# Performance work log

Measured on AMD Instinct MI355X. Metric: run time of the kernel, lower is better.

Reference implementation:

```python
import jax, jax.numpy as jnp
import numpy as np

B, C, H, W = 4, 64, 64, 64
C8 = C // 8


def cl_attention(x, gamma):
    # DANet CAM-style channel attention: [B,C,H,W] -> [B,C,H,W]
    b, c, h, w = x.shape
    xf = x.reshape(b, c, h * w)                       # b c n
    energy = jnp.einsum('bcn,bdn->bcd', xf, xf)       # b c c
    energy = jnp.max(energy, axis=-1, keepdims=True) - energy
    attn = jax.nn.softmax(energy, axis=-1)
    out = jnp.einsum('bcd,bdn->bcn', attn, xf).reshape(b, c, h, w)
    return gamma * out + x


def setup_inputs() -> dict:
    key = jax.random.key(0)
    ks = jax.random.split(key, 8)
    s = 0.02
    return {
        'cnn_feat': jax.random.normal(ks[0], (B, C, H, W), jnp.float32),
        'vit_feat': jax.random.normal(ks[1], (B, C, H, W), jnp.float32),
        'Wq': jax.random.normal(ks[2], (C8, C), jnp.float32) * s,   # 1x1 conv kernel
        'bq': jnp.zeros((C8,), jnp.float32),
        'Wk': jax.random.normal(ks[3], (C8, C), jnp.float32) * s,
        'bk': jnp.zeros((C8,), jnp.float32),
        'Wv': jax.random.normal(ks[4], (C, C), jnp.float32) * s,
        'bv': jnp.zeros((C,), jnp.float32),
        'gamma': jnp.zeros((1,), jnp.float32),
        'gamma_cla_cnn': jnp.zeros((1,), jnp.float32),
        'gamma_cla_vit': jnp.zeros((1,), jnp.float32),
    }


def reference(cnn_feat, vit_feat, Wq, bq, Wk, bk, Wv, bv, gamma,
              gamma_cla_cnn, gamma_cla_vit):
    b, c, h, w = cnn_feat.shape
    n = h * w

    cnn_att = cl_attention(cnn_feat, gamma_cla_cnn)   # b c h w
    vit_att = cl_attention(vit_feat, gamma_cla_vit)   # b c h w

    # query: 1x1 conv -> view(b, C8, n) -> permute -> (b, n, C8)
    q = jnp.einsum('bchw,oc->bhwo', cnn_att, Wq).reshape(b, n, -1) + bq

    # vit: rearrange 'b c h w -> b (h w) c'
    vit_flat = vit_att.reshape(b, c, n).transpose(0, 2, 1)          # b n c
    k = vit_flat @ Wk.T + bk                                        # b n C8
    v = vit_flat @ Wv.T + bv                                        # b n C

    energy = jnp.einsum('bqd,bkd->bqk', q, k)                       # b n n
    attn = jax.nn.softmax(energy, axis=-1)
    out = jnp.einsum('bqk,bkc->bqc', attn, v)                       # b n c
    out = out.transpose(0, 2, 1).reshape(b, c, h, w)                # 'b (h w) c -> b c h w'
    return gamma * out + cnn_feat
```

## Files before the change

kernel.cpp:

```cpp
#include <hip/hip_runtime.h>
#include <hip/hip_bf16.h>

#define BSZ 4
#define CC 64
#define NN 4096
#define CN (CC*NN)
#define BCN (BSZ*CN)

typedef __attribute__((ext_vector_type(4))) float    f4v;
typedef __attribute__((ext_vector_type(4))) int      i4v;
typedef __attribute__((ext_vector_type(2))) int      i2v;
typedef __attribute__((ext_vector_type(2))) unsigned u2v;
typedef __attribute__((ext_vector_type(8))) short    s8v;

#define DPP_F(x_, ctrl_) __builtin_bit_cast(float, \
    __builtin_amdgcn_update_dpp(0, __builtin_bit_cast(int, (float)(x_)), (ctrl_), 0xf, 0xf, true))
#define QP_X1 0xB1

__device__ __forceinline__ unsigned pack_bf16(float lo, float hi) {
    unsigned l = __builtin_bit_cast(unsigned, lo);
    unsigned h = __builtin_bit_cast(unsigned, hi);
    return (h & 0xFFFF0000u) | (l >> 16);
}
__device__ __forceinline__ unsigned pack2(float lo, float hi) {
    float2 f2; f2.x = lo; f2.y = hi;
    __hip_bfloat162 h = __float22bfloat162_rn(f2);
    unsigned u;
    __builtin_memcpy(&u, &h, 4);
    return u;
}
__device__ __forceinline__ float blo(int d) {
    return __builtin_bit_cast(float, (unsigned)d << 16);
}
__device__ __forceinline__ float bhi(int d) {
    return __builtin_bit_cast(float, (unsigned)d & 0xFFFF0000u);
}

__global__ __launch_bounds__(256) void gram_k(const float* __restrict__ cnn,
                                              const float* __restrict__ vit,
                                              float* __restrict__ part) {
    __shared__ __align__(16) float sXT[128*68];
    int t = threadIdx.x;
    int blk = blockIdx.x;
    int ch = blk & 31, b = (blk >> 5) & 3, i2 = blk >> 7;
    const float* X = (i2 ? vit : cnn) + b * CN;
    int n0 = ch * 128;
#pragma unroll
    for (int j = 0; j < 8; j++) {
        int idx = t + j * 256;
        int c = idx >> 5, n4 = idx & 31;
        f4v val = *(const f4v*)&X[c * NN + n0 + n4 * 4];
        int base = (n4 * 4) * 68 + c;
        sXT[base]       = val[0];
        sXT[base + 68]  = val[1];
        sXT[base + 136] = val[2];
        sXT[base + 204] = val[3];
    }
    __syncthreads();
    int tc = (t & 15) * 4, td = (t >> 4) * 4;
    f4v acc[4];
#pragma unroll
    for (int i = 0; i < 4; i++) acc[i] = (f4v){0.f, 0.f, 0.f, 0.f};
#pragma unroll 4
    for (int k = 0; k < 128; k++) {
        f4v a  = *(const f4v*)&sXT[k * 68 + tc];
        f4v bb = *(const f4v*)&sXT[k * 68 + td];
#pragma unroll
        for (int i = 0; i < 4; i++) acc[i] += a[i] * bb;
    }
    float* dst = part + ch * 32768 + (i2 * 4 + b) * 4096;
#pragma unroll
    for (int i = 0; i < 4; i++) *(f4v*)&dst[(tc + i) * 64 + td] = acc[i];
}

__global__ void gred_k(const float* __restrict__ part, float* __restrict__ G) {
    int row = blockIdx.x;
    int d = threadIdx.x;
    float s = 0.f;
#pragma unroll 8
    for (int ch = 0; ch < 32; ch++) s += part[ch * 32768 + row * 64 + d];
    float mn = s;
#pragma unroll
    for (int off = 1; off < 64; off <<= 1) mn = fminf(mn, __shfl_xor(mn, off));
    float e = __expf(mn - s);
    float sm = e;
#pragma unroll
    for (int off = 1; off < 64; off <<= 1) sm += __shfl_xor(sm, off);
    G[row * 64 + d] = e / sm;
}

__global__ __launch_bounds__(256) void weff_k(const float* __restrict__ G,
                                              const float* __restrict__ Wq,
                                              const float* __restrict__ Wk,
                                              const float* __restrict__ Wv,
                                              const float* __restrict__ gcnn,
                                              const float* __restrict__ gvit,
                                              ushort* __restrict__ WeffB) {
    __shared__ float sA[8192];
    __shared__ float sWt[1024];
    int t = threadIdx.x;
    int b = blockIdx.x / 5, tile = blockIdx.x % 5;
    for (int i = t; i < 4096; i += 256) {
        sA[i]        = G[b * 4096 + i];
        sA[4096 + i] = G[(4 + b) * 4096 + i];
    }
    __syncthreads();
    float gc = *gcnn, gv = *gvit;
#pragma unroll
    for (int k = 0; k < 4; k++) {
        int idx = k * 256 + t;
        int r = idx >> 6, c = idx & 63;
        const float* Wrow; const float* A; float g;
        if (tile == 0) {
            if (r < 8) { Wrow = Wq + r * 64;       A = sA;        g = gc; }
            else       { Wrow = Wk + (r - 8) * 64; A = sA + 4096; g = gv; }
        } else         { Wrow = Wv + ((tile - 1) * 16 + r) * 64; A = sA + 4096; g = gv; }
        float s = 0.f;
#pragma unroll 8
        for (int d = 0; d < 64; d++) s += Wrow[d] * A[d * 64 + c];
        sWt[idx] = g * s + Wrow[c];
    }
    __syncthreads();
    if (t < 128) {
        int frag = t >> 6, lane = t & 63, m = lane & 15, q4 = lane >> 4;
        i4v o;
#pragma unroll
        for (int p = 0; p < 4; p++) {
            int c0 = frag * 32 + q4 * 8 + 2 * p;
            o[p] = (int)pack_bf16(sWt[m * 64 + c0], sWt[m * 64 + c0 + 1]);
        }
        *(i4v*)&WeffB[(size_t)(b * 10 + tile * 2 + frag) * 512 + lane * 8] = o;
    }
}

__global__ __launch_bounds__(256) void qkv_k(const float* __restrict__ cnn,
                                             const float* __restrict__ vit,
                                             const ushort* __restrict__ WeffB,
                                             const float* __restrict__ bq,
                                             const float* __restrict__ bk,
                                             const float* __restrict__ bv,
                                             ushort* __restrict__ qb, ushort* __restrict__ kb,
                                             ushort* __restrict__ vT) {
    int t = threadIdx.x;
    int b = blockIdx.x >> 6, n0 = (blockIdx.x & 63) * 64;
    int w = t >> 6, lane = t & 63, c15 = lane & 15, q4 = lane >> 4;
    int n = n0 + w * 16 + c15;
    const float LOG2E = 1.44269504f;

    s8v A[10];
    const ushort* WB = WeffB + (size_t)b * 5120 + lane * 8;
#pragma unroll
    for (int i = 0; i < 10; i++)
        A[i] = __builtin_bit_cast(s8v, *(const i4v*)(WB + (size_t)i * 512));

    s8v Bc[2], Bv[2];
#pragma unroll
    for (int f = 0; f < 2; f++) {
        i4v pc, pv;
#pragma unroll
        for (int p = 0; p < 4; p++) {
            int c0 = f * 32 + q4 * 8 + p * 2;
            size_t a0 = (size_t)b * CN + (size_t)c0 * NN + n;
            pc[p] = (int)pack_bf16(cnn[a0], cnn[a0 + NN]);
            pv[p] = (int)pack_bf16(vit[a0], vit[a0 + NN]);
        }
        Bc[f] = __builtin_bit_cast(s8v, pc);
        Bv[f] = __builtin_bit_cast(s8v, pv);
    }

    f4v acc = *(const f4v*)(bq + (q4 & 1) * 4);
    acc = __builtin_amdgcn_mfma_f32_16x16x32_bf16(A[0], Bc[0], acc, 0, 0, 0);
    acc = __builtin_amdgcn_mfma_f32_16x16x32_bf16(A[1], Bc[1], acc, 0, 0, 0);
    if (q4 < 2) {
        unsigned d0 = pack_bf16(acc[0] * LOG2E, acc[1] * LOG2E);
        unsigned d1 = pack_bf16(acc[2] * LOG2E, acc[3] * LOG2E);
        unsigned long long v = ((unsigned long long)d1 << 32) | d0;
        *(unsigned long long*)&qb[(size_t)(b * NN + n) * 8 + q4 * 4] = v;
    }
    acc = *(const f4v*)(bk + (q4 & 1) * 4);
    acc = __builtin_amdgcn_mfma_f32_16x16x32_bf16(A[0], Bv[0], acc, 0, 0, 0);
    acc = __builtin_amdgcn_mfma_f32_16x16x32_bf16(A[1], Bv[1], acc, 0, 0, 0);
    if (q4 >= 2) {
        unsigned d0 = pack_bf16(acc[0], acc[1]), d1 = pack_bf16(acc[2], acc[3]);
        unsigned long long v = ((unsigned long long)d1 << 32) | d0;
        *(unsigned long long*)&kb[(size_t)(b * NN + n) * 8 + (q4 - 2) * 4] = v;
    }
#pragma unroll
    for (int tile = 1; tile < 5; tile++) {
        acc = *(const f4v*)(bv + (tile - 1) * 16 + q4 * 4);
        acc = __builtin_amdgcn_mfma_f32_16x16x32_bf16(A[tile * 2],     Bv[0], acc, 0, 0, 0);
        acc = __builtin_amdgcn_mfma_f32_16x16x32_bf16(A[tile * 2 + 1], Bv[1], acc, 0, 0, 0);
#pragma unroll
        for (int r = 0; r < 4; r++) {
            float other = DPP_F(acc[r], QP_X1);
            unsigned pkd = (lane & 1) ? pack_bf16(other, acc[r])
                                      : pack_bf16(acc[r], other);
            if (!(lane & 1)) {
                int row = (tile - 1) * 16 + q4 * 4 + r;
                *(unsigned*)&vT[(size_t)(b * 64 + row) * NN + n] = pkd;
            }
        }
    }
}

__global__ __launch_bounds__(256, 2) void flash_k(const ushort* __restrict__ qb,
                                                  const ushort* __restrict__ kb,
                                                  const ushort* __restrict__ vT,
                                                  ushort* __restrict__ pOT,
                                                  float* __restrict__ pl) {
    __shared__ __align__(16) ushort Vlds[2 * 64 * 72];
    int t = threadIdx.x;
    int lane = t & 63, w = t >> 6;
    int c15 = lane & 15, q4 = lane >> 4;
    int blk = blockIdx.x;
    int s = blk >> 7, b = (blk >> 5) & 3, q0 = (blk & 31) * 128;

    s8v qB[2];
#pragma unroll
    for (int g = 0; g < 2; g++) {
        i4v qa = (i4v){0, 0, 0, 0};
        if (q4 == 0)
            qa = *(const i4v*)(qb + (size_t)(b * NN + q0 + w * 32 + g * 16 + c15) * 8);
        qB[g] = __builtin_bit_cast(s8v, qa);
    }

    f4v accO[2][4];
#pragma unroll
    for (int g = 0; g < 2; g++)
#pragma unroll
        for (int nt = 0; nt < 4; nt++) accO[g][nt] = (f4v){0.f, 0.f, 0.f, 0.f};
    float lacc[2] = {0.f, 0.f};

    const ushort* kbb = kb + (size_t)b * NN * 8 + (size_t)c15 * 8;

    int r = t >> 2, chk = t & 3;
    const ushort* vsrc = vT + (size_t)(b * 64 + r) * NN + chk * 16;
    int vdstoff = r * 72 + 32 * (chk >> 1) + 4 * (chk & 1);
    int vreadoff = c15 * 72 + 8 * q4;

    int kbase = s * 1024;
    i4v bk_cur[4];
#pragma unroll
    for (int nt = 0; nt < 4; nt++)
        bk_cur[nt] = *(const i4v*)(kbb + (size_t)(kbase + nt * 16) * 8);
    i4v v0 = *(const i4v*)(vsrc + kbase);
    i4v v1 = *(const i4v*)(vsrc + kbase + 8);

#pragma unroll 2
    for (int kt = 0; kt < 16; kt++) {
        int k0 = kbase + kt * 64;
        ushort* vd = Vlds + (kt & 1) * 4608 + vdstoff;
        *(i2v*)(vd + 0)  = (i2v){v0[0], v0[1]};
        *(i2v*)(vd + 8)  = (i2v){v0[2], v0[3]};
        *(i2v*)(vd + 16) = (i2v){v1[0], v1[1]};
        *(i2v*)(vd + 24) = (i2v){v1[2], v1[3]};
        __syncthreads();

        const ushort* vb = Vlds + (kt & 1) * 4608 + vreadoff;
        i4v vA[2][4];
#pragma unroll
        for (int F = 0; F < 2; F++)
#pragma unroll
            for (int nt = 0; nt < 4; nt++)
                vA[F][nt] = *(const i4v*)(vb + nt * 16 * 72 + 32 * F);

        i4v bk_nxt[4];
        if (kt < 15) {
            v0 = *(const i4v*)(vsrc + k0 + 64);
            v1 = *(const i4v*)(vsrc + k0 + 64 + 8);
#pragma unroll
            for (int nt = 0; nt < 4; nt++)
                bk_nxt[nt] = *(const i4v*)(kbb + (size_t)(k0 + 64 + nt * 16) * 8);
        }

        f4v z = (f4v){0.f, 0.f, 0.f, 0.f};
        f4v S[2][4];
#pragma unroll
        for (int g = 0; g < 2; g++)
#pragma unroll
            for (int nt = 0; nt < 4; nt++)
                S[g][nt] = __builtin_amdgcn_mfma_f32_16x16x32_bf16(
                    __builtin_bit_cast(s8v, bk_cur[nt]), qB[g], z, 0, 0, 0);

        s8v Bp[2][2];
#pragma unroll
        for (int g = 0; g < 2; g++) {
            f4v p[4];
            float ps = 0.f;
#pragma unroll
            for (int nt = 0; nt < 4; nt++)
#pragma unroll
                for (int rr = 0; rr < 4; rr++) {
                    p[nt][rr] = __builtin_amdgcn_exp2f(S[g][nt][rr]);
                    ps += p[nt][rr];
                }
#pragma unroll
            for (int F = 0; F < 2; F++) {
                i4v bp;
                bp[0] = (int)pack2(p[2 * F][0],     p[2 * F][1]);
                bp[1] = (int)pack2(p[2 * F][2],     p[2 * F][3]);
                bp[2] = (int)pack2(p[2 * F + 1][0], p[2 * F + 1][1]);
                bp[3] = (int)pack2(p[2 * F + 1][2], p[2 * F + 1][3]);
                Bp[g][F] = __builtin_bit_cast(s8v, bp);
            }
            lacc[g] += ps;
        }

        __builtin_amdgcn_s_setprio(1);
#pragma unroll
        for (int F = 0; F < 2; F++)
#pragma unroll
            for (int g = 0; g < 2; g++)
#pragma unroll
                for (int nt = 0; nt < 4; nt++)
                    accO[g][nt] =
                        __builtin_amdgcn_mfma_f32_16x16x32_bf16(
                            __builtin_bit_cast(s8v, vA[F][nt]), Bp[g][F],
                            accO[g][nt], 0, 0, 0);
        __builtin_amdgcn_s_setprio(0);

        if (kt < 15) {
#pragma unroll
            for (int nt = 0; nt < 4; nt++) bk_cur[nt] = bk_nxt[nt];
        }
    }

#pragma unroll
    for (int g = 0; g < 2; g++) {
        lacc[g] += __shfl_xor(lacc[g], 16);
        lacc[g] += __shfl_xor(lacc[g], 32);
    }

#pragma unroll
    for (int g = 0; g < 2; g++) {
        int qg = q0 + w * 32 + g * 16 + c15;
#pragma unroll
        for (int nt = 0; nt < 4; nt++) {
            int cg = nt * 4 + q4;
            u2v d;
            d[0] = pack2(accO[g][nt][0], accO[g][nt][1]);
            d[1] = pack2(accO[g][nt][2], accO[g][nt][3]);
            *(u2v*)&pOT[((size_t)((s * 4 + b) * 16 + cg) * NN + qg) * 4] = d;
        }
        if (q4 == 0)
            pl[(size_t)(s * 4 + b) * NN + qg] = lacc[g];
    }
}

__global__ __launch_bounds__(256) void comb_k(const ushort* __restrict__ pOT,
                                              const float* __restrict__ pl,
                                              const float* __restrict__ cnn,
                                              const float* __restrict__ gamma,
                                              float* __restrict__ out) {
    int t = threadIdx.x;
    int b = blockIdx.x >> 6, n0 = (blockIdx.x & 63) * 64;
    int nq = t & 15, cl = t >> 4;
    int n = n0 + nq * 4;
    f4v L = (f4v){0.f, 0.f, 0.f, 0.f};
#pragma unroll
    for (int s = 0; s < 4; s++)
        L += *(const f4v*)&pl[(size_t)(s * 4 + b) * NN + n];
    float g = *gamma;
    f4v rv;
#pragma unroll
    for (int j = 0; j < 4; j++) rv[j] = g / L[j];

    f4v Oc[4];
#pragma unroll
    for (int cc = 0; cc < 4; cc++) Oc[cc] = (f4v){0.f, 0.f, 0.f, 0.f};
#pragma unroll
    for (int s = 0; s < 4; s++) {
        const ushort* src = pOT + ((size_t)((s * 4 + b) * 16 + cl) * NN + n) * 4;
        i4v a  = *(const i4v*)src;
        i4v bb = *(const i4v*)(src + 8);
        Oc[0][0] += blo(a[0]);  Oc[1][0] += bhi(a[0]);
        Oc[2][0] += blo(a[1]);  Oc[3][0] += bhi(a[1]);
        Oc[0][1] += blo(a[2]);  Oc[1][1] += bhi(a[2]);
        Oc[2][1] += blo(a[3]);  Oc[3][1] += bhi(a[3]);
        Oc[0][2] += blo(bb[0]); Oc[1][2] += bhi(bb[0]);
        Oc[2][2] += blo(bb[1]); Oc[3][2] += bhi(bb[1]);
        Oc[0][3] += blo(bb[2]); Oc[1][3] += bhi(bb[2]);
        Oc[2][3] += blo(bb[3]); Oc[3][3] += bhi(bb[3]);
    }
#pragma unroll
    for (int cc = 0; cc < 4; cc++) {
        size_t gi = (size_t)(b * 64 + cl * 4 + cc) * NN + n;
        f4v cv = *(const f4v*)&cnn[gi];
        *(f4v*)&out[gi] = Oc[cc] * rv + cv;
    }
}

extern "C" void kernel_launch(void* const* d_in, const int* in_sizes, int n_in,
                              void* d_out, int out_size, void* d_ws, size_t ws_size,
                              hipStream_t stream) {
    const float* cnn  = (const float*)d_in[0];
    const float* vit  = (const float*)d_in[1];
    const float* Wq   = (const float*)d_in[2];
    const float* bq   = (const float*)d_in[3];
    const float* Wk   = (const float*)d_in[4];
    const float* bk   = (const float*)d_in[5];
    const float* Wv   = (const float*)d_in[6];
    const float* bv   = (const float*)d_in[7];
    const float* gam  = (const float*)d_in[8];
    const float* gcnn = (const float*)d_in[9];
    const float* gvit = (const float*)d_in[10];
    float* out = (float*)d_out;

    float* ws = (float*)d_ws;
    ushort* pOT   = (ushort*)ws;
    float*  part  = ws;
    float*  G     = ws + 8388608;
    ushort* WeffB = (ushort*)(ws + 8421376);
    ushort* qb    = (ushort*)(ws + 8431616);
    ushort* kb    = (ushort*)(ws + 8497152);
    ushort* vT    = (ushort*)(ws + 8562688);
    float*  pl    = ws + 9086976;

    gram_k <<<256, 256, 0, stream>>>(cnn, vit, part);
    gred_k <<<512, 64,  0, stream>>>(part, G);
    weff_k <<<20,  256, 0, stream>>>(G, Wq, Wk, Wv, gcnn, gvit, WeffB);
    qkv_k  <<<256, 256, 0, stream>>>(cnn, vit, WeffB, bq, bk, bv, qb, kb, vT);
    flash_k<<<512, 256, 0, stream>>>(qb, kb, vT, pOT, pl);
    comb_k <<<256, 256, 0, stream>>>(pOT, pl, cnn, gam, out);
}
```

Before: 126.6 us.

## Fuse prologue kernels with grid barriers and merge flash attention with combine

The gram, reduce, weight-fold and QKV projection kernels are merged into one persistent 256-block kernel that separates stages with atomic-counter grid barriers. The flash kernel now uses 512 threads and splits keys across two in-block halves, reducing the partial outputs through shared memory. It then writes the gamma-scaled result plus residual directly, which removes the bf16 partial-output buffer and the separate combine kernel. This saves several launches and a global round trip, but the grid barriers rely on all 256 blocks being co-resident, and the final stores are strided per element.

```diff
diff --git a/kernel.cpp b/kernel.cpp
--- a/kernel.cpp
+++ b/kernel.cpp
@@ -10,7 +10,6 @@
 typedef __attribute__((ext_vector_type(4))) float    f4v;
 typedef __attribute__((ext_vector_type(4))) int      i4v;
 typedef __attribute__((ext_vector_type(2))) int      i2v;
-typedef __attribute__((ext_vector_type(2))) unsigned u2v;
 typedef __attribute__((ext_vector_type(8))) short    s8v;
 
 #define DPP_F(x_, ctrl_) __builtin_bit_cast(float, \
@@ -29,234 +28,245 @@
     __builtin_memcpy(&u, &h, 4);
     return u;
 }
-__device__ __forceinline__ float blo(int d) {
-    return __builtin_bit_cast(float, (unsigned)d << 16);
-}
-__device__ __forceinline__ float bhi(int d) {
-    return __builtin_bit_cast(float, (unsigned)d & 0xFFFF0000u);
-}
-
-__global__ __launch_bounds__(256) void gram_k(const float* __restrict__ cnn,
-                                              const float* __restrict__ vit,
-                                              float* __restrict__ part) {
-    __shared__ __align__(16) float sXT[128*68];
+
+__device__ __forceinline__ void gsync(unsigned* ctr, unsigned target) {
+    __syncthreads();
+    if (threadIdx.x == 0) {
+        __threadfence();
+        atomicAdd(ctr, 1u);
+        while (__hip_atomic_load(ctr, __ATOMIC_ACQUIRE,
+                                 __HIP_MEMORY_SCOPE_AGENT) < target)
+            __builtin_amdgcn_s_sleep(2);
+        __threadfence();
+    }
+    __syncthreads();
+}
+
+__global__ __launch_bounds__(256) void fused_a(
+        const float* __restrict__ cnn, const float* __restrict__ vit,
+        const float* __restrict__ Wq,  const float* __restrict__ Wk,
+        const float* __restrict__ Wv,
+        const float* __restrict__ gcnn, const float* __restrict__ gvit,
+        const float* __restrict__ bq,  const float* __restrict__ bk,
+        const float* __restrict__ bv,
+        float* __restrict__ part, float* __restrict__ G,
+        ushort* __restrict__ WeffB,
+        ushort* __restrict__ qb, ushort* __restrict__ kb,
+        ushort* __restrict__ vT, unsigned* __restrict__ ctr) {
+    __shared__ __align__(16) float smem[9216];
     int t = threadIdx.x;
     int blk = blockIdx.x;
-    int ch = blk & 31, b = (blk >> 5) & 3, i2 = blk >> 7;
-    const float* X = (i2 ? vit : cnn) + b * CN;
-    int n0 = ch * 128;
-#pragma unroll
-    for (int j = 0; j < 8; j++) {
-        int idx = t + j * 256;
-        int c = idx >> 5, n4 = idx & 31;
-        f4v val = *(const f4v*)&X[c * NN + n0 + n4 * 4];
-        int base = (n4 * 4) * 68 + c;
-        sXT[base]       = val[0];
-        sXT[base + 68]  = val[1];
-        sXT[base + 136] = val[2];
-        sXT[base + 204] = val[3];
-    }
-    __syncthreads();
-    int tc = (t & 15) * 4, td = (t >> 4) * 4;
-    f4v acc[4];
-#pragma unroll
-    for (int i = 0; i < 4; i++) acc[i] = (f4v){0.f, 0.f, 0.f, 0.f};
+
+    {
+        float* sXT = smem;
+        int ch = blk & 31, b = (blk >> 5) & 3, i2 = blk >> 7;
+        const float* X = (i2 ? vit : cnn) + b * CN;
+        int n0 = ch * 128;
+#pragma unroll
+        for (int j = 0; j < 8; j++) {
+            int idx = t + j * 256;
+            int c = idx >> 5, n4 = idx & 31;
+            f4v val = *(const f4v*)&X[c * NN + n0 + n4 * 4];
+            int base = (n4 * 4) * 68 + c;
+            sXT[base]       = val[0];
+            sXT[base + 68]  = val[1];
+            sXT[base + 136] = val[2];
+            sXT[base + 204] = val[3];
+        }
+        __syncthreads();
+        int tc = (t & 15) * 4, td = (t >> 4) * 4;
+        f4v acc[4];
+#pragma unroll
+        for (int i = 0; i < 4; i++) acc[i] = (f4v){0.f, 0.f, 0.f, 0.f};
 #pragma unroll 4
-    for (int k = 0; k < 128; k++) {
-        f4v a  = *(const f4v*)&sXT[k * 68 + tc];
-        f4v bb = *(const f4v*)&sXT[k * 68 + td];
-#pragma unroll
-        for (int i = 0; i < 4; i++) acc[i] += a[i] * bb;
-    }
-    float* dst = part + ch * 32768 + (i2 * 4 + b) * 4096;
-#pragma unroll
-    for (int i = 0; i < 4; i++) *(f4v*)&dst[(tc + i) * 64 + td] = acc[i];
-}
-
-__global__ void gred_k(const float* __restrict__ part, float* __restrict__ G) {
-    int row = blockIdx.x;
-    int d = threadIdx.x;
-    float s = 0.f;
+        for (int k = 0; k < 128; k++) {
+            f4v a  = *(const f4v*)&sXT[k * 68 + tc];
+            f4v bb = *(const f4v*)&sXT[k * 68 + td];
+#pragma unroll
+            for (int i = 0; i < 4; i++) acc[i] += a[i] * bb;
+        }
+        float* dst = part + ch * 32768 + (i2 * 4 + b) * 4096;
+#pragma unroll
+        for (int i = 0; i < 4; i++) *(f4v*)&dst[(tc + i) * 64 + td] = acc[i];
+    }
+    gsync(ctr, 256);
+
+    {
+        int w = t >> 6, d = t & 63;
+        int row = blk * 2 + (w & 1), hf = w >> 1;
+        float s = 0.f;
+#pragma unroll
+        for (int ch = hf * 16; ch < hf * 16 + 16; ch++)
+            s += part[ch * 32768 + row * 64 + d];
+        smem[w * 64 + d] = s;
+        __syncthreads();
+        if (w < 2) {
+            int r = blk * 2 + w;
+            float sv = smem[w * 64 + d] + smem[(w + 2) * 64 + d];
+            float mn = sv;
+#pragma unroll
+            for (int off = 1; off < 64; off <<= 1) mn = fminf(mn, __shfl_xor(mn, off));
+            float e = __expf(mn - sv);
+            float sm2 = e;
+#pragma unroll
+            for (int off = 1; off < 64; off <<= 1) sm2 += __shfl_xor(sm2, off);
+            G[r * 64 + d] = e / sm2;
+        }
+    }
+    gsync(ctr, 512);
+
+    if (blk < 20) {
+        float* sA = smem;
+        float* sWt = smem + 8192;
+        int b = blk / 5, tile = blk % 5;
+        for (int i = t; i < 4096; i += 256) {
+            sA[i]        = G[b * 4096 + i];
+            sA[4096 + i] = G[(4 + b) * 4096 + i];
+        }
+        __syncthreads();
+        float gc = *gcnn, gv = *gvit;
+#pragma unroll
+        for (int k = 0; k < 4; k++) {
+            int idx = k * 256 + t;
+            int r = idx >> 6, c = idx & 63;
+            const float* Wrow; const float* A; float g;
+            if (tile == 0) {
+                if (r < 8) { Wrow = Wq + r * 64;       A = sA;        g = gc; }
+                else       { Wrow = Wk + (r - 8) * 64; A = sA + 4096; g = gv; }
+            } else         { Wrow = Wv + ((tile - 1) * 16 + r) * 64; A = sA + 4096; g = gv; }
+            float s = 0.f;
 #pragma unroll 8
-    for (int ch = 0; ch < 32; ch++) s += part[ch * 32768 + row * 64 + d];
-    float mn = s;
-#pragma unroll
-    for (int off = 1; off < 64; off <<= 1) mn = fminf(mn, __shfl_xor(mn, off));
-    float e = __expf(mn - s);
-    float sm = e;
-#pragma unroll
-    for (int off = 1; off < 64; off <<= 1) sm += __shfl_xor(sm, off);
-    G[row * 64 + d] = e / sm;
-}
-
-__global__ __launch_bounds__(256) void weff_k(const float* __restrict__ G,
-                                              const float* __restrict__ Wq,
-                                              const float* __restrict__ Wk,
-                                              const float* __restrict__ Wv,
-                                              const float* __restrict__ gcnn,
-                                              const float* __restrict__ gvit,
-                                              ushort* __restrict__ WeffB) {
-    __shared__ float sA[8192];
-    __shared__ float sWt[1024];
-    int t = threadIdx.x;
-    int b = blockIdx.x / 5, tile = blockIdx.x % 5;
-    for (int i = t; i < 4096; i += 256) {
-        sA[i]        = G[b * 4096 + i];
-        sA[4096 + i] = G[(4 + b) * 4096 + i];
-    }
-    __syncthreads();
-    float gc = *gcnn, gv = *gvit;
-#pragma unroll
-    for (int k = 0; k < 4; k++) {
-        int idx = k * 256 + t;
-        int r = idx >> 6, c = idx & 63;
-        const float* Wrow; const float* A; float g;
-        if (tile == 0) {
-            if (r < 8) { Wrow = Wq + r * 64;       A = sA;        g = gc; }
-            else       { Wrow = Wk + (r - 8) * 64; A = sA + 4096; g = gv; }
-        } else         { Wrow = Wv + ((tile - 1) * 16 + r) * 64; A = sA + 4096; g = gv; }
-        float s = 0.f;
-#pragma unroll 8
-        for (int d = 0; d < 64; d++) s += Wrow[d] * A[d * 64 + c];
-        sWt[idx] = g * s + Wrow[c];
-    }
-    __syncthreads();
-    if (t < 128) {
-        int frag = t >> 6, lane = t & 63, m = lane & 15, q4 = lane >> 4;
-        i4v o;
-#pragma unroll
-        for (int p = 0; p < 4; p++) {
-            int c0 = frag * 32 + q4 * 8 + 2 * p;
-            o[p] = (int)pack_bf16(sWt[m * 64 + c0], sWt[m * 64 + c0 + 1]);
-        }
-        *(i4v*)&WeffB[(size_t)(b * 10 + tile * 2 + frag) * 512 + lane * 8] = o;
-    }
-}
-
-__global__ __launch_bounds__(256) void qkv_k(const float* __restrict__ cnn,
-                                             const float* __restrict__ vit,
-                                             const ushort* __restrict__ WeffB,
-                                             const float* __restrict__ bq,
-                                             const float* __restrict__ bk,
-                                             const float* __restrict__ bv,
-                                             ushort* __restrict__ qb, ushort* __restrict__ kb,
-                                             ushort* __restrict__ vT) {
-    int t = threadIdx.x;
-    int b = blockIdx.x >> 6, n0 = (blockIdx.x & 63) * 64;
-    int w = t >> 6, lane = t & 63, c15 = lane & 15, q4 = lane >> 4;
-    int n = n0 + w * 16 + c15;
-    const float LOG2E = 1.44269504f;
-
-    s8v A[10];
-    const ushort* WB = WeffB + (size_t)b * 5120 + lane * 8;
-#pragma unroll
-    for (int i = 0; i < 10; i++)
-        A[i] = __builtin_bit_cast(s8v, *(const i4v*)(WB + (size_t)i * 512));
-
-    s8v Bc[2], Bv[2];
-#pragma unroll
-    for (int f = 0; f < 2; f++) {
-        i4v pc, pv;
-#pragma unroll
-        for (int p = 0; p < 4; p++) {
-            int c0 = f * 32 + q4 * 8 + p * 2;
-            size_t a0 = (size_t)b * CN + (size_t)c0 * NN + n;
-            pc[p] = (int)pack_bf16(cnn[a0], cnn[a0 + NN]);
-            pv[p] = (int)pack_bf16(vit[a0], vit[a0 + NN]);
-        }
-        Bc[f] = __builtin_bit_cast(s8v, pc);
-        Bv[f] = __builtin_bit_cast(s8v, pv);
-    }
-
-    f4v acc = *(const f4v*)(bq + (q4 & 1) * 4);
-    acc = __builtin_amdgcn_mfma_f32_16x16x32_bf16(A[0], Bc[0], acc, 0, 0, 0);
-    acc = __builtin_amdgcn_mfma_f32_16x16x32_bf16(A[1], Bc[1], acc, 0, 0, 0);
-    if (q4 < 2) {
-        unsigned d0 = pack_bf16(acc[0] * LOG2E, acc[1] * LOG2E);
-        unsigned d1 = pack_bf16(acc[2] * LOG2E, acc[3] * LOG2E);
-        unsigned long long v = ((unsigned long long)d1 << 32) | d0;
-        *(unsigned long long*)&qb[(size_t)(b * NN + n) * 8 + q4 * 4] = v;
-    }
-    acc = *(const f4v*)(bk + (q4 & 1) * 4);
-    acc = __builtin_amdgcn_mfma_f32_16x16x32_bf16(A[0], Bv[0], acc, 0, 0, 0);
-    acc = __builtin_amdgcn_mfma_f32_16x16x32_bf16(A[1], Bv[1], acc, 0, 0, 0);
-    if (q4 >= 2) {
-        unsigned d0 = pack_bf16(acc[0], acc[1]), d1 = pack_bf16(acc[2], acc[3]);
-        unsigned long long v = ((unsigned long long)d1 << 32) | d0;
-        *(unsigned long long*)&kb[(size_t)(b * NN + n) * 8 + (q4 - 2) * 4] = v;
-    }
-#pragma unroll
-    for (int tile = 1; tile < 5; tile++) {
-        acc = *(const f4v*)(bv + (tile - 1) * 16 + q4 * 4);
-        acc = __builtin_amdgcn_mfma_f32_16x16x32_bf16(A[tile * 2],     Bv[0], acc, 0, 0, 0);
-        acc = __builtin_amdgcn_mfma_f32_16x16x32_bf16(A[tile * 2 + 1], Bv[1], acc, 0, 0, 0);
-#pragma unroll
-        for (int r = 0; r < 4; r++) {
-            float other = DPP_F(acc[r], QP_X1);
-            unsigned pkd = (lane & 1) ? pack_bf16(other, acc[r])
-                                      : pack_bf16(acc[r], other);
-            if (!(lane & 1)) {
-                int row = (tile - 1) * 16 + q4 * 4 + r;
-                *(unsigned*)&vT[(size_t)(b * 64 + row) * NN + n] = pkd;
-            }
-        }
-    }
-}
-
-__global__ __launch_bounds__(256, 2) void flash_k(const ushort* __restrict__ qb,
-                                                  const ushort* __restrict__ kb,
-                                                  const ushort* __restrict__ vT,
-                                                  ushort* __restrict__ pOT,
-                                                  float* __restrict__ pl) {
-    __shared__ __align__(16) ushort Vlds[2 * 64 * 72];
+            for (int d = 0; d < 64; d++) s += Wrow[d] * A[d * 64 + c];
+            sWt[idx] = g * s + Wrow[c];
+        }
+        __syncthreads();
+        if (t < 128) {
+            int frag = t >> 6, lane = t & 63, m = lane & 15, q4 = lane >> 4;
+            i4v o;
+#pragma unroll
+            for (int p = 0; p < 4; p++) {
+                int c0 = frag * 32 + q4 * 8 + 2 * p;
+                o[p] = (int)pack_bf16(sWt[m * 64 + c0], sWt[m * 64 + c0 + 1]);
+            }
+            *(i4v*)&WeffB[(size_t)(b * 10 + tile * 2 + frag) * 512 + lane * 8] = o;
+        }
+    }
+    gsync(ctr, 768);
+
+    {
+        int b = blk >> 6, n0 = (blk & 63) * 64;
+        int w = t >> 6, lane = t & 63, c15 = lane & 15, q4 = lane >> 4;
+        int n = n0 + w * 16 + c15;
+        const float LOG2E = 1.44269504f;
+
+        s8v A[10];
+        const ushort* WB = WeffB + (size_t)b * 5120 + lane * 8;
+#pragma unroll
+        for (int i = 0; i < 10; i++)
+            A[i] = __builtin_bit_cast(s8v, *(const i4v*)(WB + (size_t)i * 512));
+
+        s8v Bc[2], Bv[2];
+#pragma unroll
+        for (int f = 0; f < 2; f++) {
+            i4v pc, pv;
+#pragma unroll
+            for (int p = 0; p < 4; p++) {
+                int c0 = f * 32 + q4 * 8 + p * 2;
+                size_t a0 = (size_t)b * CN + (size_t)c0 * NN + n;
+                pc[p] = (int)pack_bf16(cnn[a0], cnn[a0 + NN]);
+                pv[p] = (int)pack_bf16(vit[a0], vit[a0 + NN]);
+            }
+            Bc[f] = __builtin_bit_cast(s8v, pc);
+            Bv[f] = __builtin_bit_cast(s8v, pv);
+        }
+
+        f4v acc = *(const f4v*)(bq + (q4 & 1) * 4);
+        acc = __builtin_amdgcn_mfma_f32_16x16x32_bf16(A[0], Bc[0], acc, 0, 0, 0);
+        acc = __builtin_amdgcn_mfma_f32_16x16x32_bf16(A[1], Bc[1], acc, 0, 0, 0);
+        if (q4 < 2) {
+            unsigned d0 = pack_bf16(acc[0] * LOG2E, acc[1] * LOG2E);
+            unsigned d1 = pack_bf16(acc[2] * LOG2E, acc[3] * LOG2E);
+            unsigned long long v = ((unsigned long long)d1 << 32) | d0;
+            *(unsigned long long*)&qb[(size_t)(b * NN + n) * 8 + q4 * 4] = v;
+        }
+        acc = *(const f4v*)(bk + (q4 & 1) * 4);
+        acc = __builtin_amdgcn_mfma_f32_16x16x32_bf16(A[0], Bv[0], acc, 0, 0, 0);
+        acc = __builtin_amdgcn_mfma_f32_16x16x32_bf16(A[1], Bv[1], acc, 0, 0, 0);
+        if (q4 >= 2) {
+            unsigned d0 = pack_bf16(acc[0], acc[1]), d1 = pack_bf16(acc[2], acc[3]);
+            unsigned long long v = ((unsigned long long)d1 << 32) | d0;
+            *(unsigned long long*)&kb[(size_t)(b * NN + n) * 8 + (q4 - 2) * 4] = v;
+        }
+#pragma unroll
+        for (int tile = 1; tile < 5; tile++) {
+            acc = *(const f4v*)(bv + (tile - 1) * 16 + q4 * 4);
+            acc = __builtin_amdgcn_mfma_f32_16x16x32_bf16(A[tile * 2],     Bv[0], acc, 0, 0, 0);
+            acc = __builtin_amdgcn_mfma_f32_16x16x32_bf16(A[tile * 2 + 1], Bv[1], acc, 0, 0, 0);
+#pragma unroll
+            for (int r = 0; r < 4; r++) {
+                float other = DPP_F(acc[r], QP_X1);
+                unsigned pkd = (lane & 1) ? pack_bf16(other, acc[r])
+                                          : pack_bf16(acc[r], other);
+                if (!(lane & 1)) {
+                    int row = (tile - 1) * 16 + q4 * 4 + r;
+                    *(unsigned*)&vT[(size_t)(b * 64 + row) * NN + n] = pkd;
+                }
+            }
+        }
+    }
+}
+
+__global__ __launch_bounds__(512, 2) void flashc_k(
+        const ushort* __restrict__ qb, const ushort* __restrict__ kb,
+        const ushort* __restrict__ vT, const float* __restrict__ cnn,
+        const float* __restrict__ gamma, float* __restrict__ out) {
+    __shared__ __align__(16) ushort Vlds[4 * 4608];
+    __shared__ float sO[4 * 16 * 64];
+    __shared__ float sL[4 * 64];
+
     int t = threadIdx.x;
     int lane = t & 63, w = t >> 6;
     int c15 = lane & 15, q4 = lane >> 4;
     int blk = blockIdx.x;
-    int s = blk >> 7, b = (blk >> 5) & 3, q0 = (blk & 31) * 128;
-
-    s8v qB[2];
-#pragma unroll
-    for (int g = 0; g < 2; g++) {
-        i4v qa = (i4v){0, 0, 0, 0};
-        if (q4 == 0)
-            qa = *(const i4v*)(qb + (size_t)(b * NN + q0 + w * 32 + g * 16 + c15) * 8);
-        qB[g] = __builtin_bit_cast(s8v, qa);
-    }
-
-    f4v accO[2][4];
-#pragma unroll
-    for (int g = 0; g < 2; g++)
-#pragma unroll
-        for (int nt = 0; nt < 4; nt++) accO[g][nt] = (f4v){0.f, 0.f, 0.f, 0.f};
-    float lacc[2] = {0.f, 0.f};
+    int b = blk >> 6, q0 = (blk & 63) * 64;
+    int wq = w & 3, half = w >> 2;
+
+    i4v qa = (i4v){0, 0, 0, 0};
+    if (q4 == 0)
+        qa = *(const i4v*)(qb + (size_t)(b * NN + q0 + wq * 16 + c15) * 8);
+    s8v qB = __builtin_bit_cast(s8v, qa);
+
+    f4v accO[4];
+#pragma unroll
+    for (int nt = 0; nt < 4; nt++) accO[nt] = (f4v){0.f, 0.f, 0.f, 0.f};
+    float lacc = 0.f;
 
     const ushort* kbb = kb + (size_t)b * NN * 8 + (size_t)c15 * 8;
-
-    int r = t >> 2, chk = t & 3;
-    const ushort* vsrc = vT + (size_t)(b * 64 + r) * NN + chk * 16;
-    int vdstoff = r * 72 + 32 * (chk >> 1) + 4 * (chk & 1);
+    int kbase = half * 2048;
+
+    int stile = t >> 8;
+    int sr = (t >> 2) & 63, schk = t & 3;
+    const ushort* vsrc = vT + (size_t)(b * 64 + sr) * NN + stile * 2048 + schk * 16;
+    int vdstoff = sr * 72 + 32 * (schk >> 1) + 4 * (schk & 1);
     int vreadoff = c15 * 72 + 8 * q4;
 
-    int kbase = s * 1024;
     i4v bk_cur[4];
 #pragma unroll
     for (int nt = 0; nt < 4; nt++)
         bk_cur[nt] = *(const i4v*)(kbb + (size_t)(kbase + nt * 16) * 8);
-    i4v v0 = *(const i4v*)(vsrc + kbase);
-    i4v v1 = *(const i4v*)(vsrc + kbase + 8);
+    i4v v0 = *(const i4v*)(vsrc);
+    i4v v1 = *(const i4v*)(vsrc + 8);
 
 #pragma unroll 2
-    for (int kt = 0; kt < 16; kt++) {
-        int k0 = kbase + kt * 64;
-        ushort* vd = Vlds + (kt & 1) * 4608 + vdstoff;
+    for (int kt = 0; kt < 32; kt++) {
+        ushort* vd = Vlds + (stile * 2 + (kt & 1)) * 4608 + vdstoff;
         *(i2v*)(vd + 0)  = (i2v){v0[0], v0[1]};
         *(i2v*)(vd + 8)  = (i2v){v0[2], v0[3]};
         *(i2v*)(vd + 16) = (i2v){v1[0], v1[1]};
         *(i2v*)(vd + 24) = (i2v){v1[2], v1[3]};
         __syncthreads();
 
-        const ushort* vb = Vlds + (kt & 1) * 4608 + vreadoff;
+        const ushort* vb = Vlds + (half * 2 + (kt & 1)) * 4608 + vreadoff;
         i4v vA[2][4];
 #pragma unroll
         for (int F = 0; F < 2; F++)
@@ -265,128 +275,82 @@
                 vA[F][nt] = *(const i4v*)(vb + nt * 16 * 72 + 32 * F);
 
         i4v bk_nxt[4];
-        if (kt < 15) {
-            v0 = *(const i4v*)(vsrc + k0 + 64);
-            v1 = *(const i4v*)(vsrc + k0 + 64 + 8);
+        if (kt < 31) {
+            v0 = *(const i4v*)(vsrc + (kt + 1) * 64);
+            v1 = *(const i4v*)(vsrc + (kt + 1) * 64 + 8);
 #pragma unroll
             for (int nt = 0; nt < 4; nt++)
-                bk_nxt[nt] = *(const i4v*)(kbb + (size_t)(k0 + 64 + nt * 16) * 8);
+                bk_nxt[nt] = *(const i4v*)(kbb +
+                    (size_t)(kbase + (kt + 1) * 64 + nt * 16) * 8);
         }
 
         f4v z = (f4v){0.f, 0.f, 0.f, 0.f};
-        f4v S[2][4];
-#pragma unroll
-        for (int g = 0; g < 2; g++)
+        f4v S[4];
+#pragma unroll
+        for (int nt = 0; nt < 4; nt++)
+            S[nt] = __builtin_amdgcn_mfma_f32_16x16x32_bf16(
+                __builtin_bit_cast(s8v, bk_cur[nt]), qB, z, 0, 0, 0);
+
+        f4v p[4];
+        float ps = 0.f;
+#pragma unroll
+        for (int nt = 0; nt < 4; nt++)
+#pragma unroll
+            for (int rr = 0; rr < 4; rr++) {
+                p[nt][rr] = __builtin_amdgcn_exp2f(S[nt][rr]);
+                ps += p[nt][rr];
+            }
+        lacc += ps;
+        s8v Bp[2];
+#pragma unroll
+        for (int F = 0; F < 2; F++) {
+            i4v bp;
+            bp[0] = (int)pack2(p[2 * F][0],     p[2 * F][1]);
+            bp[1] = (int)pack2(p[2 * F][2],     p[2 * F][3]);
+            bp[2] = (int)pack2(p[2 * F + 1][0], p[2 * F + 1][1]);
+            bp[3] = (int)pack2(p[2 * F + 1][2], p[2 * F + 1][3]);
+            Bp[F] = __builtin_bit_cast(s8v, bp);
+        }
+
+        __builtin_amdgcn_s_setprio(1);
+#pragma unroll
+        for (int F = 0; F < 2; F++)
 #pragma unroll
             for (int nt = 0; nt < 4; nt++)
-                S[g][nt] = __builtin_amdgcn_mfma_f32_16x16x32_bf16(
-                    __builtin_bit_cast(s8v, bk_cur[nt]), qB[g], z, 0, 0, 0);
-
-        s8v Bp[2][2];
-#pragma unroll
-        for (int g = 0; g < 2; g++) {
-            f4v p[4];
-            float ps = 0.f;
-#pragma unroll
-            for (int nt = 0; nt < 4; nt++)
-#pragma unroll
-                for (int rr = 0; rr < 4; rr++) {
-                    p[nt][rr] = __builtin_amdgcn_exp2f(S[g][nt][rr]);
-                    ps += p[nt][rr];
-                }
-#pragma unroll
-            for (int F = 0; F < 2; F++) {
-                i4v bp;
-                bp[0] = (int)pack2(p[2 * F][0],     p[2 * F][1]);
-                bp[1] = (int)pack2(p[2 * F][2],     p[2 * F][3]);
-                bp[2] = (int)pack2(p[2 * F + 1][0], p[2 * F + 1][1]);
-                bp[3] = (int)pack2(p[2 * F + 1][2], p[2 * F + 1][3]);
-                Bp[g][F] = __builtin_bit_cast(s8v, bp);
-            }
-            lacc[g] += ps;
-        }
-
-        __builtin_amdgcn_s_setprio(1);
-#pragma unroll
-        for (int F = 0; F < 2; F++)
-#pragma unroll
-            for (int g = 0; g < 2; g++)
-#pragma unroll
-                for (int nt = 0; nt < 4; nt++)
-                    accO[g][nt] =
-                        __builtin_amdgcn_mfma_f32_16x16x32_bf16(
-                            __builtin_bit_cast(s8v, vA[F][nt]), Bp[g][F],
-                            accO[g][nt], 0, 0, 0);
+                accO[nt] = __builtin_amdgcn_mfma_f32_16x16x32_bf16(
+                    __builtin_bit_cast(s8v, vA[F][nt]), Bp[F], accO[nt], 0, 0, 0);
         __builtin_amdgcn_s_setprio(0);
 
-        if (kt < 15) {
+        if (kt < 31) {
 #pragma unroll
             for (int nt = 0; nt < 4; nt++) bk_cur[nt] = bk_nxt[nt];
         }
     }
 
-#pragma unroll
-    for (int g = 0; g < 2; g++) {
-        lacc[g] += __shfl_xor(lacc[g], 16);
-        lacc[g] += __shfl_xor(lacc[g], 32);
-    }
-
-#pragma unroll
-    for (int g = 0; g < 2; g++) {
-        int qg = q0 + w * 32 + g * 16 + c15;
-#pragma unroll
-        for (int nt = 0; nt < 4; nt++) {
-            int cg = nt * 4 + q4;
-            u2v d;
-            d[0] = pack2(accO[g][nt][0], accO[g][nt][1]);
-            d[1] = pack2(accO[g][nt][2], accO[g][nt][3]);
-            *(u2v*)&pOT[((size_t)((s * 4 + b) * 16 + cg) * NN + qg) * 4] = d;
-        }
-        if (q4 == 0)
-            pl[(size_t)(s * 4 + b) * NN + qg] = lacc[g];
-    }
-}
-
-__global__ __launch_bounds__(256) void comb_k(const ushort* __restrict__ pOT,
-                                              const float* __restrict__ pl,
-                                              const float* __restrict__ cnn,
-                                              const float* __restrict__ gamma,
-                                              float* __restrict__ out) {
-    int t = threadIdx.x;
-    int b = blockIdx.x >> 6, n0 = (blockIdx.x & 63) * 64;
-    int nq = t & 15, cl = t >> 4;
-    int n = n0 + nq * 4;
-    f4v L = (f4v){0.f, 0.f, 0.f, 0.f};
-#pragma unroll
-    for (int s = 0; s < 4; s++)
-        L += *(const f4v*)&pl[(size_t)(s * 4 + b) * NN + n];
-    float g = *gamma;
-    f4v rv;
-#pragma unroll
-    for (int j = 0; j < 4; j++) rv[j] = g / L[j];
-
-    f4v Oc[4];
-#pragma unroll
-    for (int cc = 0; cc < 4; cc++) Oc[cc] = (f4v){0.f, 0.f, 0.f, 0.f};
-#pragma unroll
-    for (int s = 0; s < 4; s++) {
-        const ushort* src = pOT + ((size_t)((s * 4 + b) * 16 + cl) * NN + n) * 4;
-        i4v a  = *(const i4v*)src;
-        i4v bb = *(const i4v*)(src + 8);
-        Oc[0][0] += blo(a[0]);  Oc[1][0] += bhi(a[0]);
-        Oc[2][0] += blo(a[1]);  Oc[3][0] += bhi(a[1]);
-        Oc[0][1] += blo(a[2]);  Oc[1][1] += bhi(a[2]);
-        Oc[2][1] += blo(a[3]);  Oc[3][1] += bhi(a[3]);
-        Oc[0][2] += blo(bb[0]); Oc[1][2] += bhi(bb[0]);
-        Oc[2][2] += blo(bb[1]); Oc[3][2] += bhi(bb[1]);
-        Oc[0][3] += blo(bb[2]); Oc[1][3] += bhi(bb[2]);
-        Oc[2][3] += blo(bb[3]); Oc[3][3] += bhi(bb[3]);
-    }
-#pragma unroll
-    for (int cc = 0; cc < 4; cc++) {
-        size_t gi = (size_t)(b * 64 + cl * 4 + cc) * NN + n;
-        f4v cv = *(const f4v*)&cnn[gi];
-        *(f4v*)&out[gi] = Oc[cc] * rv + cv;
+    lacc += __shfl_xor(lacc, 16);
+    lacc += __shfl_xor(lacc, 32);
+
+    if (half == 1) {
+#pragma unroll
+        for (int nt = 0; nt < 4; nt++)
+#pragma unroll
+            for (int rr = 0; rr < 4; rr++)
+                sO[(wq * 16 + nt * 4 + rr) * 64 + lane] = accO[nt][rr];
+        sL[wq * 64 + lane] = lacc;
+    }
+    __syncthreads();
+    if (half == 0) {
+        lacc += sL[wq * 64 + lane];
+        float rv = *gamma / lacc;
+#pragma unroll
+        for (int nt = 0; nt < 4; nt++)
+#pragma unroll
+            for (int rr = 0; rr < 4; rr++) {
+                float o = accO[nt][rr] + sO[(wq * 16 + nt * 4 + rr) * 64 + lane];
+                int c = nt * 16 + q4 * 4 + rr;
+                size_t gi = (size_t)(b * 64 + c) * NN + q0 + wq * 16 + c15;
+                out[gi] = o * rv + cnn[gi];
+            }
     }
 }
 
@@ -407,19 +371,16 @@
     float* out = (float*)d_out;
 
     float* ws = (float*)d_ws;
-    ushort* pOT   = (ushort*)ws;
-    float*  part  = ws;
-    float*  G     = ws + 8388608;
-    ushort* WeffB = (ushort*)(ws + 8421376);
-    ushort* qb    = (ushort*)(ws + 8431616);
-    ushort* kb    = (ushort*)(ws + 8497152);
-    ushort* vT    = (ushort*)(ws + 8562688);
-    float*  pl    = ws + 9086976;
-
-    gram_k <<<256, 256, 0, stream>>>(cnn, vit, part);
-    gred_k <<<512, 64,  0, stream>>>(part, G);
-    weff_k <<<20,  256, 0, stream>>>(G, Wq, Wk, Wv, gcnn, gvit, WeffB);
-    qkv_k  <<<256, 256, 0, stream>>>(cnn, vit, WeffB, bq, bk, bv, qb, kb, vT);
-    flash_k<<<512, 256, 0, stream>>>(qb, kb, vT, pOT, pl);
-    comb_k <<<256, 256, 0, stream>>>(pOT, pl, cnn, gam, out);
-}
+    float*    part  = ws;
+    float*    G     = ws + 1048576;
+    ushort*   WeffB = (ushort*)(ws + 1081344);
+    ushort*   qb    = (ushort*)(ws + 1091584);
+    ushort*   kb    = (ushort*)(ws + 1157120);
+    ushort*   vT    = (ushort*)(ws + 1222656);
+    unsigned* ctr   = (unsigned*)(ws + 1746944);
+
+    hipMemsetAsync(ctr, 0, 4, stream);
+    fused_a<<<256, 256, 0, stream>>>(cnn, vit, Wq, Wk, Wv, gcnn, gvit,
+                                     bq, bk, bv, part, G, WeffB, qb, kb, vT, ctr);
+    flashc_k<<<256, 512, 0, stream>>>(qb, kb, vT, cnn, gam, out);
+}
```

After: 216.1 us. +70.7%, slower.
